# Kernel optimization log

Hardware: AMD Instinct MI355X
Metric: run time of the kernel (lower is better)

Reference implementation:

```python
import jax, jax.numpy as jnp
import numpy as np
from jax import lax

VOCAB = 32000
EMBED = 1024
HIDDEN = 1024
ML = 64          # config.MAX_LENGTH
L = 50           # input sentence length
HH = HIDDEN // 2 # per-direction encoder hidden


def _lstm_cell(x, h, c, Wih, Whh, bih, bhh):
    # torch LSTM gate order: i, f, g, o
    g = x @ Wih.T + h @ Whh.T + bih + bhh
    i, f, gg, o = jnp.split(g, 4)
    i = jax.nn.sigmoid(i)
    f = jax.nn.sigmoid(f)
    gg = jnp.tanh(gg)
    o = jax.nn.sigmoid(o)
    c = f * c + i * gg
    return o * jnp.tanh(c), c


def setup_inputs() -> dict:
    key = jax.random.key(0)
    ks = jax.random.split(key, 24)
    def n(k, shape, s=0.05):
        return jax.random.normal(k, shape, jnp.float32) * s
    return {
        "x_tokens": jax.random.randint(ks[0], (L,), 0, VOCAB, jnp.int32),
        "allowed_mask": jnp.ones((VOCAB + ML,), jnp.float32),
        "embedding": n(ks[1], (VOCAB, EMBED)),
        # encoder bi-LSTM (two cells, each hidden//2)
        "Wih_f": n(ks[2], (4 * HH, EMBED)), "Whh_f": n(ks[3], (4 * HH, HH)),
        "bih_f": n(ks[4], (4 * HH,)), "bhh_f": n(ks[5], (4 * HH,)),
        "Wih_b": n(ks[6], (4 * HH, EMBED)), "Whh_b": n(ks[7], (4 * HH, HH)),
        "bih_b": n(ks[8], (4 * HH,)), "bhh_b": n(ks[9], (4 * HH,)),
        # decoder LSTM: input = embed + 2*hidden
        "Wih_d": n(ks[10], (4 * HIDDEN, EMBED + 2 * HIDDEN)),
        "Whh_d": n(ks[11], (4 * HIDDEN, HIDDEN)),
        "bih_d": n(ks[12], (4 * HIDDEN,)), "bhh_d": n(ks[13], (4 * HIDDEN,)),
        # attention: Linear(2*hidden -> MAX_LENGTH)
        "attn_W": n(ks[14], (ML, 2 * HIDDEN)), "attn_b": n(ks[15], (ML,)),
        # generate layer: Linear(hidden -> vocab)
        "gen_W": n(ks[16], (VOCAB, HIDDEN)), "gen_b": n(ks[17], (VOCAB,)),
        # copy layer: Linear(hidden -> hidden)
        "copy_W": n(ks[18], (HIDDEN, HIDDEN)), "copy_b": n(ks[19], (HIDDEN,)),
    }


def _forward(allowed_mask, embedding, Wih_f, Whh_f, bih_f, bhh_f,
             Wih_b, Whh_b, bih_b, bhh_b, Wih_d, Whh_d, bih_d, bhh_d,
             attn_W, attn_b, gen_W, gen_b, copy_W, copy_b, x_tokens):
    xemb = embedding[x_tokens]  # (L, EMBED)

    # --- encoder: two LSTM cells both stepped forward-in-time (as in the
    # original, where the bidirectional LSTM is called one token at a time) ---
    def enc_step(carry, xe):
        hf, cf, hb, cb = carry
        hf, cf = _lstm_cell(xe, hf, cf, Wih_f, Whh_f, bih_f, bhh_f)
        hb, cb = _lstm_cell(xe, hb, cb, Wih_b, Whh_b, bih_b, bhh_b)
        return (hf, cf, hb, cb), jnp.concatenate([hf, hb])

    z = jnp.zeros((HH,), xemb.dtype)
    (hf, cf, hb, cb), enc = lax.scan(enc_step, (z, z, z, z), xemb)
    enc_outs = jnp.zeros((ML, HIDDEN), xemb.dtype).at[:L].set(enc)  # padded buffer
    h0 = jnp.concatenate([hf, hb])  # (HIDDEN,) decoder init
    c0 = jnp.concatenate([cf, cb])

    copy_enc = jnp.tanh(enc_outs @ copy_W.T + copy_b)  # (ML, HIDDEN), loop-invariant
    pos = jnp.arange(ML)
    sent_pad = jnp.full((ML,), -1, jnp.int32).at[:L].set(x_tokens)
    sos_emb = embedding[0]

    def dec_step(carry, t):
        h, c, prev_probs, prev_word, dec_in = carry
        first = t == 0
        # attentive read
        a = jnp.concatenate([dec_in, h])  # (2*HIDDEN,)
        attw = jax.nn.softmax(a @ attn_W.T + attn_b)
        attentive = attw @ enc_outs  # (HIDDEN,)
        # selective (copy) read from previous step's copy probs
        pc = prev_probs[VOCAB:]
        m = ((pos >= 1) & (pos < L - 1) & (sent_pad != prev_word)).astype(pc.dtype)
        pc = pc * m
        s = pc.sum()
        pc = jnp.where(s > 0, pc / jnp.where(s > 0, s, 1.0), pc)
        selective = pc @ enc_outs
        zero = jnp.zeros_like(attentive)
        attentive = jnp.where(first, zero, attentive)
        selective = jnp.where(first, zero, selective)
        # decoder LSTM step
        h, c = _lstm_cell(jnp.concatenate([dec_in, selective, attentive]),
                          h, c, Wih_d, Whh_d, bih_d, bhh_d)
        gen = h @ gen_W.T + gen_b        # (VOCAB,)
        copy = copy_enc @ h              # (ML,)
        probs = jax.nn.softmax(jnp.concatenate([gen, copy]))
        dist = probs * allowed_mask
        # deterministic action (argmax in place of Categorical.sample)
        aidx = jnp.argmax(dist)
        is_voc = aidx < VOCAB
        src = sent_pad[jnp.clip(aidx - VOCAB, 0, L - 1)]
        action = jnp.where(is_voc, aidx, src).astype(jnp.int32)
        prob = dist[aidx] + jnp.where(
            is_voc, jnp.zeros((), dist.dtype), dist[jnp.clip(action, 0, VOCAB - 1)])
        new = (h, c, lax.stop_gradient(probs), action, embedding[action])
        return new, (h, prob, action)

    carry0 = (h0, c0, jnp.zeros((VOCAB + ML,), h0.dtype),
              jnp.array(-1, jnp.int32), sos_emb)
    _, (hs, probs, actions) = lax.scan(dec_step, carry0, jnp.arange(ML))
    states = jnp.concatenate([h0[None], hs])  # (ML+1, HIDDEN)
    return states, probs, actions


def reference(x_tokens, allowed_mask, embedding, Wih_f, Whh_f, bih_f, bhh_f,
              Wih_b, Whh_b, bih_b, bhh_b, Wih_d, Whh_d, bih_d, bhh_d,
              attn_W, attn_b, gen_W, gen_b, copy_W, copy_b):
    return _forward(allowed_mask, embedding, Wih_f, Whh_f, bih_f, bhh_f,
                    Wih_b, Whh_b, bih_b, bhh_b, Wih_d, Whh_d, bih_d, bhh_d,
                    attn_W, attn_b, gen_W, gen_b, copy_W, copy_b, x_tokens)
```

## Files before the change

### kernel.cpp

```cpp
#include <hip/hip_runtime.h>
#include <math.h>

#define L 50
#define ML 64
#define VOCAB 32000
#define EMBED 1024
#define HID 1024
#define HH 512
#define TOT (VOCAB+ML)
#define NPART 501

#define WS_ENC_GATES 0
#define WS_C_ENC     8192
#define WS_ENC_OUTS  10240
#define WS_COPY_ENC  75776
#define WS_H_DEC     141312
#define WS_C_DEC     143360
#define WS_X_DEC     145408
#define WS_DGATES    148480
#define WS_LOGITS    152576
#define WS_PARTS     184640
#define WS_ATTW      186688
#define WS_PC        186752
#define WS_ACT       186816
#define WS_G         186880
#define WS_G_END     (186880+8192*64)
#define WS_PREG      711168
#define WS_PREG_END  (711168+50*4096)
#define WS_AH        915968
#define WS_P         916032
#define WS_P_END     (916032+32000*64)

__device__ __forceinline__ float wred_sum(float v){
  #pragma unroll
  for(int o=32;o;o>>=1) v += __shfl_xor(v,o,64);
  return v;
}
__device__ __forceinline__ float wred_max(float v){
  #pragma unroll
  for(int o=32;o;o>>=1) v = fmaxf(v,__shfl_xor(v,o,64));
  return v;
}
__device__ __forceinline__ float sigm(float x){ return 1.0f/(1.0f+__expf(-x)); }
__device__ __forceinline__ float d4(float4 a, float4 b){ return a.x*b.x + a.y*b.y + a.z*b.z + a.w*b.w; }

__global__ __launch_bounds__(256) void k_enc_pre2(
  const int* __restrict__ xt, const float* __restrict__ emb,
  const float* __restrict__ Wih_f, const float* __restrict__ bih_f, const float* __restrict__ bhh_f,
  const float* __restrict__ Wih_b, const float* __restrict__ bih_b, const float* __restrict__ bhh_b,
  float* __restrict__ ws)
{
  __shared__ int toks[L];
  const int tid=threadIdx.x, b=blockIdx.x, wave=tid>>6, lane=tid&63;
  float* pg = ws + WS_PREG;
  if(tid<L) toks[tid]=xt[tid];
  float4 wih[2][4]; float bias[2];
  #pragma unroll
  for(int rr=0;rr<2;rr++){
    int r=b*8+wave*2+rr; bool isF=(r<2048); int rl=isF?r:(r-2048);
    const float* wp=(isF?Wih_f:Wih_b)+(size_t)rl*EMBED;
    #pragma unroll
    for(int c4=0;c4<4;c4++) wih[rr][c4]=*(const float4*)(wp+c4*256+lane*4);
    bias[rr]= isF?(bih_f[rl]+bhh_f[rl]):(bih_b[rl]+bhh_b[rl]);
  }
  __syncthreads();
  const float* er0 = emb + (size_t)toks[0]*EMBED;
  float4 e0=*(const float4*)(er0      +lane*4);
  float4 e1=*(const float4*)(er0+256  +lane*4);
  float4 e2=*(const float4*)(er0+512  +lane*4);
  float4 e3=*(const float4*)(er0+768  +lane*4);
  for(int t=0;t<L;t++){
    int tn = (t+1<L)? t+1 : t;
    const float* en = emb + (size_t)toks[tn]*EMBED;
    float4 n0=*(const float4*)(en      +lane*4);
    float4 n1=*(const float4*)(en+256  +lane*4);
    float4 n2=*(const float4*)(en+512  +lane*4);
    float4 n3=*(const float4*)(en+768  +lane*4);
    #pragma unroll
    for(int rr=0;rr<2;rr++){
      int r=b*8+wave*2+rr;
      float acc = d4(wih[rr][0],e0)+d4(wih[rr][1],e1)+d4(wih[rr][2],e2)+d4(wih[rr][3],e3);
      acc=wred_sum(acc);
      if(lane==0) pg[(size_t)t*4096+r]=acc+bias[rr];
    }
    e0=n0; e1=n1; e2=n2; e3=n3;
  }
}

__global__ __launch_bounds__(256) void k_enc_rec(
  const float* __restrict__ Whh_f, const float* __restrict__ Whh_b,
  float* __restrict__ ws, int t)
{
  __shared__ __align__(16) float h_lds[1024];
  const int tid=threadIdx.x, b=blockIdx.x, wave=tid>>6, lane=tid&63;
  float* gates   = ws + WS_ENC_GATES;
  float* c_enc   = ws + WS_C_ENC;
  float* enc_outs= ws + WS_ENC_OUTS;
  const float* pg = ws + WS_PREG + (size_t)t*4096;
  if(t>0){
    const float* gp = gates + ((t-1)&1)*4096;
    const float* cp = c_enc + (t&1)*1024;
    float* cw = c_enc + ((t-1)&1)*1024;
    for(int u=tid;u<1024;u+=256){
      int base=(u<512)?0:2048, uu=(u<512)?u:(u-512);
      float ig=gp[base+uu], fg=gp[base+512+uu], gg=gp[base+1024+uu], og=gp[base+1536+uu];
      float cprev=(t==1)?0.0f:cp[u];
      float c=sigm(fg)*cprev+sigm(ig)*tanhf(gg);
      float h=sigm(og)*tanhf(c);
      h_lds[u]=h;
      if(b==0){ cw[u]=c; enc_outs[(size_t)(t-1)*1024+u]=h; }
    }
  }
  __syncthreads();
  float* gw = gates + (t&1)*4096;
  #pragma unroll
  for(int rr=0;rr<2;rr++){
    int r=b*8+wave*2+rr; bool isF=(r<2048); int rl=isF?r:(r-2048);
    if(t==0){
      if(lane==0) gw[r]=pg[r];
    } else {
      const float* hr=(isF?Whh_f:Whh_b)+(size_t)rl*HH;
      const float* hs=&h_lds[isF?0:512];
      float acc=0.0f;
      #pragma unroll
      for(int c2=0;c2<2;c2++){
        int m=c2*256+lane*4;
        acc += d4(*(const float4*)(hr+m), *(const float4*)(&hs[m]));
      }
      acc=wred_sum(acc);
      if(lane==0) gw[r]=pg[r]+acc;
    }
  }
}

__global__ __launch_bounds__(256) void k_enc_step(
  const int* __restrict__ xt, const float* __restrict__ emb,
  const float* __restrict__ Wih_f, const float* __restrict__ Whh_f,
  const float* __restrict__ bih_f, const float* __restrict__ bhh_f,
  const float* __restrict__ Wih_b, const float* __restrict__ Whh_b,
  const float* __restrict__ bih_b, const float* __restrict__ bhh_b,
  float* __restrict__ ws, int t)
{
  __shared__ __align__(16) float h_lds[1024];
  __shared__ __align__(16) float xe[1024];
  const int tid = threadIdx.x;
  float* gates   = ws + WS_ENC_GATES;
  float* c_enc   = ws + WS_C_ENC;
  float* enc_outs= ws + WS_ENC_OUTS;
  {
    const int tok = xt[t];
    const float* er = emb + (size_t)tok*EMBED;
    for(int j=tid;j<1024;j+=256) xe[j]=er[j];
  }
  if(t>0){
    const float* gp = gates + ((t-1)&1)*4096;
    const float* cp = c_enc + (t&1)*1024;
    float* cw = c_enc + ((t-1)&1)*1024;
    for(int u=tid;u<1024;u+=256){
      int base=(u<512)?0:2048, uu=(u<512)?u:(u-512);
      float ig=gp[base+uu], fg=gp[base+512+uu], gg=gp[base+1024+uu], og=gp[base+1536+uu];
      float cprev=(t==1)?0.0f:cp[u];
      float c=sigm(fg)*cprev+sigm(ig)*tanhf(gg);
      float h=sigm(og)*tanhf(c);
      h_lds[u]=h;
      if(blockIdx.x==0){ cw[u]=c; enc_outs[(size_t)(t-1)*1024+u]=h; }
    }
  }
  __syncthreads();
  float* gw = gates + (t&1)*4096;
  const int wave=tid>>6, lane=tid&63;
  for(int rr=0;rr<2;rr++){
    int r=blockIdx.x*8+wave*2+rr;
    bool isF=(r<2048); int rl=isF?r:(r-2048);
    const float* Wih=isF?Wih_f:Wih_b;
    const float* Whh=isF?Whh_f:Whh_b;
    float bias=isF?(bih_f[rl]+bhh_f[rl]):(bih_b[rl]+bhh_b[rl]);
    const float* wr=Wih+(size_t)rl*EMBED;
    float acc=0.0f;
    #pragma unroll
    for(int c4=0;c4<4;c4++){
      int m=c4*256+lane*4;
      acc += d4(*(const float4*)(wr+m), *(const float4*)(&xe[m]));
    }
    if(t>0){
      const float* hr=Whh+(size_t)rl*HH;
      const float* hs=&h_lds[isF?0:512];
      #pragma unroll
      for(int c2=0;c2<2;c2++){
        int m=c2*256+lane*4;
        acc += d4(*(const float4*)(hr+m), *(const float4*)(&hs[m]));
      }
    }
    acc=wred_sum(acc);
    if(lane==0) gw[r]=acc+bias;
  }
}

__global__ __launch_bounds__(256) void k_copy_final(
  const float* __restrict__ emb,
  const float* __restrict__ copy_W, const float* __restrict__ copy_b,
  float* __restrict__ ws, float* __restrict__ out)
{
  __shared__ __align__(16) float hf[1024];
  const int tid=threadIdx.x, b=blockIdx.x, wave=tid>>6, lane=tid&63;
  float* gates = ws + WS_ENC_GATES;
  float* c_enc = ws + WS_C_ENC;
  float* enc_outs = ws + WS_ENC_OUTS;
  float* cenc = ws + WS_COPY_ENC;
  float* h_dec = ws + WS_H_DEC;
  float* c_dec = ws + WS_C_DEC;
  float* x_dec = ws + WS_X_DEC;
  {
    const float* gp = gates + ((L-1)&1)*4096;
    const float* cp = c_enc + ((L-2)&1)*1024;
    for(int u=tid;u<1024;u+=256){
      int base=(u<512)?0:2048, uu=(u<512)?u:(u-512);
      float ig=gp[base+uu], fg=gp[base+512+uu], gg=gp[base+1024+uu], og=gp[base+1536+uu];
      float c=sigm(fg)*cp[u]+sigm(ig)*tanhf(gg);
      float h=sigm(og)*tanhf(c);
      hf[u]=h;
      if(b==0){
        enc_outs[(size_t)(L-1)*1024+u]=h;
        h_dec[1024+u]=h;
        c_dec[1024+u]=c;
        out[u]=h;
      }
    }
    if(b==1) for(int j=tid;j<(ML-L)*1024;j+=256) enc_outs[(size_t)L*1024+j]=0.0f;
    if(b==2) for(int j=tid;j<1024;j+=256){
      x_dec[j]=emb[j];
      x_dec[1024+j]=0.0f;
      x_dec[2048+j]=0.0f;
    }
  }
  __syncthreads();
  int j = b*4 + wave;
  const float* wr = copy_W + (size_t)j*1024;
  float4 w0=*(const float4*)(wr+0*256+lane*4);
  float4 w1=*(const float4*)(wr+1*256+lane*4);
  float4 w2=*(const float4*)(wr+2*256+lane*4);
  float4 w3=*(const float4*)(wr+3*256+lane*4);
  float bj = copy_b[j];
  for(int k=0;k<L-1;k++){
    const float* er = enc_outs + (size_t)k*1024;
    float acc = d4(w0,*(const float4*)(er+0*256+lane*4))
              + d4(w1,*(const float4*)(er+1*256+lane*4))
              + d4(w2,*(const float4*)(er+2*256+lane*4))
              + d4(w3,*(const float4*)(er+3*256+lane*4));
    acc = wred_sum(acc);
    if(lane==0) cenc[(size_t)k*1024+j]=tanhf(acc+bj);
  }
  {
    float acc = d4(w0,*(const float4*)(&hf[0*256+lane*4]))
              + d4(w1,*(const float4*)(&hf[1*256+lane*4]))
              + d4(w2,*(const float4*)(&hf[2*256+lane*4]))
              + d4(w3,*(const float4*)(&hf[3*256+lane*4]));
    acc = wred_sum(acc);
    if(lane==0) cenc[(size_t)(L-1)*1024+j]=tanhf(acc+bj);
  }
  if(lane==0){
    float z=tanhf(0.0f+bj);
    for(int k=L;k<ML;k++) cenc[(size_t)k*1024+j]=z;
  }
}

__global__ __launch_bounds__(256) void k_gmat3(const float* __restrict__ Wih_d, float* __restrict__ ws)
{
  const int tid=threadIdx.x, wave=tid>>6, lane=tid&63;
  const float* enc = ws + WS_ENC_OUTS;
  float* G = ws + WS_G;
  float4 w[4][4];
  int rg[4];
  #pragma unroll
  for(int q=0;q<4;q++){
    int r = blockIdx.x*16 + wave*4 + q;
    rg[q]=r;
    const float* W = (r<4096) ? (Wih_d + (size_t)r*3072 + 1024)
                              : (Wih_d + (size_t)(r-4096)*3072 + 2048);
    #pragma unroll
    for(int c4=0;c4<4;c4++) w[q][c4]=*(const float4*)(W + c4*256 + lane*4);
  }
  const float* er0 = enc;
  float4 e0=*(const float4*)(er0      +lane*4);
  float4 e1=*(const float4*)(er0+256  +lane*4);
  float4 e2=*(const float4*)(er0+512  +lane*4);
  float4 e3=*(const float4*)(er0+768  +lane*4);
  for(int k=0;k<L;k++){
    int kn = (k+1<L)? k+1 : k;
    const float* en = enc + (size_t)kn*1024;
    float4 n0=*(const float4*)(en      +lane*4);
    float4 n1=*(const float4*)(en+256  +lane*4);
    float4 n2=*(const float4*)(en+512  +lane*4);
    float4 n3=*(const float4*)(en+768  +lane*4);
    #pragma unroll
    for(int q=0;q<4;q++){
      float acc = d4(w[q][0],e0)+d4(w[q][1],e1)+d4(w[q][2],e2)+d4(w[q][3],e3);
      acc=wred_sum(acc);
      if(lane==0) G[(size_t)rg[q]*64 + k]=acc;
    }
    e0=n0; e1=n1; e2=n2; e3=n3;
  }
  if(lane==0){
    #pragma unroll
    for(int q=0;q<4;q++)
      for(int kk=L;kk<64;kk++) G[(size_t)rg[q]*64 + kk]=0.0f;
  }
}

__global__ __launch_bounds__(256) void k_pmat3(
  const float* __restrict__ emb, const float* __restrict__ attn_W, float* __restrict__ ws)
{
  const int tid=threadIdx.x, wave=tid>>6, lane=tid&63;
  float* P = ws + WS_P;
  const int w0 = (blockIdx.x>>2)*16;
  const int r0 = (blockIdx.x&3)*16 + wave*4;
  float4 w[4][4];
  #pragma unroll
  for(int q=0;q<4;q++){
    const float* wr = attn_W + (size_t)(r0+q)*2048;
    #pragma unroll
    for(int c4=0;c4<4;c4++) w[q][c4]=*(const float4*)(wr + c4*256 + lane*4);
  }
  const float* er0 = emb + (size_t)w0*EMBED;
  float4 e0=*(const float4*)(er0      +lane*4);
  float4 e1=*(const float4*)(er0+256  +lane*4);
  float4 e2=*(const float4*)(er0+512  +lane*4);
  float4 e3=*(const float4*)(er0+768  +lane*4);
  for(int wv=0;wv<16;wv++){
    int wn = (wv+1<16)? wv+1 : wv;
    const float* en = emb + (size_t)(w0+wn)*EMBED;
    float4 n0=*(const float4*)(en      +lane*4);
    float4 n1=*(const float4*)(en+256  +lane*4);
    float4 n2=*(const float4*)(en+512  +lane*4);
    float4 n3=*(const float4*)(en+768  +lane*4);
    #pragma unroll
    for(int q=0;q<4;q++){
      float acc = d4(w[q][0],e0)+d4(w[q][1],e1)+d4(w[q][2],e2)+d4(w[q][3],e3);
      acc=wred_sum(acc);
      if(lane==0) P[(size_t)(w0+wv)*64 + r0+q]=acc;
    }
    e0=n0; e1=n1; e2=n2; e3=n3;
  }
}

__global__ __launch_bounds__(256) void k_fin16(
  const int* __restrict__ xt, const float* __restrict__ amask,
  const float* __restrict__ emb,
  const float* __restrict__ attn_W, const float* __restrict__ attn_b,
  float* __restrict__ ws, float* __restrict__ out, int t, int fin_only)
{
  __shared__ __align__(16) float dec_in[1024];
  __shared__ __align__(16) float hprev[1024];
  __shared__ float r_lm[256], r_sm[256], r_ky[256];
  __shared__ int r_ix[256];
  __shared__ float s_lmax, s_Z;
  __shared__ int s_act;
  const int tid=threadIdx.x, b=blockIdx.x, wave=tid>>6, lane=tid&63;
  float* h_dec=ws+WS_H_DEC;
  float* logits=ws+WS_LOGITS; float* parts=ws+WS_PARTS;
  float* attw_raw=ws+WS_ATTW; float* pcw=ws+WS_PC;
  {
    float lm=-INFINITY, sm=0.0f, ky=-INFINITY; int ix=0x7fffffff;
    for(int i=tid;i<NPART;i+=256){
      const float4 p = *(const float4*)(parts+(size_t)i*4);
      float plm=p.x, psm=p.y, pky=p.z; int pix=__float_as_int(p.w);
      if(plm>lm){ sm = sm*__expf(lm-plm)+psm; lm=plm; }
      else sm += psm*__expf(plm-lm);
      if(pky>ky || (pky==ky && pix<ix)){ ky=pky; ix=pix; }
    }
    r_lm[tid]=lm; r_sm[tid]=sm; r_ky[tid]=ky; r_ix[tid]=ix;
    __syncthreads();
    for(int s=128;s;s>>=1){
      if(tid<s){
        float blm=r_lm[tid+s], bsm=r_sm[tid+s];
        float alm=r_lm[tid], a_sm=r_sm[tid];
        if(blm>alm){ r_sm[tid]=a_sm*__expf(alm-blm)+bsm; r_lm[tid]=blm; }
        else r_sm[tid]=a_sm+bsm*__expf(blm-alm);
        float bky=r_ky[tid+s]; int bix=r_ix[tid+s];
        if(bky>r_ky[tid] || (bky==r_ky[tid] && bix<r_ix[tid])){ r_ky[tid]=bky; r_ix[tid]=bix; }
      }
      __syncthreads();
    }
    if(tid==0){
      float lmax=r_lm[0]; float Z=r_sm[0];
      float bky=r_ky[0];
      int aidx = (bky==-INFINITY)?0:r_ix[0];
      bool isv = aidx<VOCAB;
      int kcl = aidx-VOCAB; kcl = kcl<0?0:(kcl>(L-1)?(L-1):kcl);
      int sp = xt[kcl];
      int action = isv? aidx : sp;
      if(b==0){
        float prob = amask[aidx]*__expf(logits[aidx]-lmax)/Z;
        if(!isv){
          int a2 = action<0?0:(action>(VOCAB-1)?(VOCAB-1):action);
          prob += amask[a2]*__expf(logits[a2]-lmax)/Z;
        }
        out[65*1024 + (t-1)] = prob;
        out[65*1024 + 64 + (t-1)] = (float)action;
        *(int*)(ws+WS_ACT) = action;
      }
      s_lmax=lmax; s_Z=Z; s_act=action;
    }
  }
  __syncthreads();
  if(fin_only) return;

  const int action = s_act;
  if(b==0 && tid<64){
    int k=tid;
    float v=__expf(logits[VOCAB+k]-s_lmax)/s_Z;
    int sp=(k<L)? xt[k] : -1;
    float m=(k>=1 && k<(L-1) && sp!=action)?1.0f:0.0f;
    float pv=v*m;
    float s=wred_sum(pv);
    pcw[k]=(s>0.0f)? pv/s : pv;
  }
  {
    int row = action<0 ? action+VOCAB : action;
    const float* er = emb + (size_t)row*EMBED;
    const float* hp = h_dec + ((t-1)&1)*1024;
    for(int j=tid;j<1024;j+=256){ dec_in[j]=er[j]; hprev[j]=hp[j]; }
  }
  __syncthreads();
  {
    int r = b*4 + wave;
    const float* wr = attn_W + (size_t)r*2048;
    float acc=0.0f;
    #pragma unroll
    for(int c4=0;c4<4;c4++){
      int m=c4*256+lane*4;
      acc += d4(*(const float4*)(wr+m),      *(const float4*)(&dec_in[m]));
      acc += d4(*(const float4*)(wr+1024+m), *(const float4*)(&hprev[m]));
    }
    acc=wred_sum(acc);
    if(lane==0) attw_raw[r]=acc+attn_b[r];
  }
}

__global__ __launch_bounds__(256) void k_dec_gates4(
  const int* __restrict__ xt, const float* __restrict__ amask,
  const float* __restrict__ emb, const float* __restrict__ attn_b,
  const float* __restrict__ Wih_d, const float* __restrict__ Whh_d,
  const float* __restrict__ bih_d, const float* __restrict__ bhh_d,
  float* __restrict__ ws, float* __restrict__ out, int t)
{
  __shared__ __align__(16) float di[1024];
  __shared__ __align__(16) float hh[1024];
  __shared__ float pcs[64], aws[64];
  __shared__ float r_lm[256], r_sm[256], r_ky[256];
  __shared__ int r_ix[256];
  __shared__ float s_lmax, s_Z;
  __shared__ int s_act;
  const int tid=threadIdx.x, b=blockIdx.x, wave=tid>>6, lane=tid&63;
  float* h_dec=ws+WS_H_DEC; float* dg=ws+WS_DGATES;
  float* logits=ws+WS_LOGITS; float* parts=ws+WS_PARTS;
  const float* G=ws+WS_G;

  if(t==0){
    for(int j=tid;j<1024;j+=256) di[j]=emb[j];
    if(tid<64){ pcs[tid]=0.0f; aws[tid]=0.0f; }
  } else {
    float lm=-INFINITY, sm=0.0f, ky=-INFINITY; int ix=0x7fffffff;
    for(int i=tid;i<NPART;i+=256){
      const float4 p = *(const float4*)(parts+(size_t)i*4);
      float plm=p.x, psm=p.y, pky=p.z; int pix=__float_as_int(p.w);
      if(plm>lm){ sm = sm*__expf(lm-plm)+psm; lm=plm; }
      else sm += psm*__expf(plm-lm);
      if(pky>ky || (pky==ky && pix<ix)){ ky=pky; ix=pix; }
    }
    r_lm[tid]=lm; r_sm[tid]=sm; r_ky[tid]=ky; r_ix[tid]=ix;
    __syncthreads();
    for(int s=128;s;s>>=1){
      if(tid<s){
        float blm=r_lm[tid+s], bsm=r_sm[tid+s];
        float alm=r_lm[tid], a_sm=r_sm[tid];
        if(blm>alm){ r_sm[tid]=a_sm*__expf(alm-blm)+bsm; r_lm[tid]=blm; }
        else r_sm[tid]=a_sm+bsm*__expf(blm-alm);
        float bky=r_ky[tid+s]; int bix=r_ix[tid+s];
        if(bky>r_ky[tid] || (bky==r_ky[tid] && bix<r_ix[tid])){ r_ky[tid]=bky; r_ix[tid]=bix; }
      }
      __syncthreads();
    }
    if(tid==0){
      float lmax=r_lm[0]; float Z=r_sm[0];
      float bky=r_ky[0];
      int aidx = (bky==-INFINITY)?0:r_ix[0];
      bool isv = aidx<VOCAB;
      int kcl = aidx-VOCAB; kcl = kcl<0?0:(kcl>(L-1)?(L-1):kcl);
      int sp = xt[kcl];
      int action = isv? aidx : sp;
      if(b==0){
        float prob = amask[aidx]*__expf(logits[aidx]-lmax)/Z;
        if(!isv){
          int a2 = action<0?0:(action>(VOCAB-1)?(VOCAB-1):action);
          prob += amask[a2]*__expf(logits[a2]-lmax)/Z;
        }
        out[65*1024 + (t-1)] = prob;
        out[65*1024 + 64 + (t-1)] = (float)action;
      }
      s_lmax=lmax; s_Z=Z; s_act=action;
    }
    __syncthreads();
    const int action = s_act;
    if(tid<64){
      int k=tid;
      float v=__expf(logits[VOCAB+k]-s_lmax)/s_Z;
      int sp=(k<L)? xt[k] : -1;
      float m=(k>=1 && k<(L-1) && sp!=action)?1.0f:0.0f;
      float pv=v*m;
      float s=wred_sum(pv);
      pcs[k]=(s>0.0f)? pv/s : pv;
    }
    __syncthreads();
    if(tid<64){
      float raw = (ws+WS_P)[(size_t)action*64 + tid] + (ws+WS_AH)[tid] + attn_b[tid];
      float mx=wred_max(raw);
      float e=__expf(raw-mx);
      float s=wred_sum(e);
      aws[tid]=e/s;
    }
    {
      const float* er = emb + (size_t)action*EMBED;
      for(int j=tid;j<1024;j+=256) di[j]=er[j];
    }
  }
  {
    const float* hp=h_dec+((t+1)&1)*1024;
    for(int j=tid;j<1024;j+=256) hh[j]=hp[j];
  }
  __syncthreads();
  for(int rr=0;rr<2;rr++){
    int r=b*8+wave*2+rr;
    const float* wd=Wih_d+(size_t)r*3072;
    float acc=0.0f;
    #pragma unroll
    for(int c4=0;c4<4;c4++){
      int m=c4*256+lane*4;
      acc += d4(*(const float4*)(wd+m), *(const float4*)(&di[m]));
    }
    const float* hr=Whh_d+(size_t)r*1024;
    #pragma unroll
    for(int c4=0;c4<4;c4++){
      int m=c4*256+lane*4;
      acc += d4(*(const float4*)(hr+m), *(const float4*)(&hh[m]));
    }
    acc += G[(size_t)r*64+lane]*pcs[lane];
    acc += G[(size_t)(4096+r)*64+lane]*aws[lane];
    acc=wred_sum(acc);
    if(lane==0) dg[r]=acc+bih_d[r]+bhh_d[r];
  }
}

__global__ __launch_bounds__(256) void k_dec_gates3(
  const float* __restrict__ emb,
  const float* __restrict__ Wih_d, const float* __restrict__ Whh_d,
  const float* __restrict__ bih_d, const float* __restrict__ bhh_d,
  float* __restrict__ ws, int t)
{
  __shared__ __align__(16) float di[1024];
  __shared__ __align__(16) float hh[1024];
  __shared__ float pcs[64], aws[64];
  const int tid=threadIdx.x;
  float* h_dec=ws+WS_H_DEC; float* dg=ws+WS_DGATES;
  const float* G=ws+WS_G;
  if(t==0){
    for(int j=tid;j<1024;j+=256) di[j]=emb[j];
    if(tid<64){ pcs[tid]=0.0f; aws[tid]=0.0f; }
  } else {
    const int action = *(const int*)(ws+WS_ACT);
    const float* er = emb + (size_t)action*EMBED;
    for(int j=tid;j<1024;j+=256) di[j]=er[j];
    if(tid<64){
      pcs[tid]=(ws+WS_PC)[tid];
      float v=(ws+WS_ATTW)[tid];
      float mx=wred_max(v);
      float e=__expf(v-mx);
      float s=wred_sum(e);
      aws[tid]=e/s;
    }
  }
  {
    const float* hp=h_dec+((t+1)&1)*1024;
    for(int j=tid;j<1024;j+=256) hh[j]=hp[j];
  }
  __syncthreads();
  const int wave=tid>>6, lane=tid&63;
  for(int rr=0;rr<2;rr++){
    int r=blockIdx.x*8+wave*2+rr;
    const float* wd=Wih_d+(size_t)r*3072;
    float acc=0.0f;
    #pragma unroll
    for(int c4=0;c4<4;c4++){
      int m=c4*256+lane*4;
      acc += d4(*(const float4*)(wd+m), *(const float4*)(&di[m]));
    }
    const float* hr=Whh_d+(size_t)r*1024;
    #pragma unroll
    for(int c4=0;c4<4;c4++){
      int m=c4*256+lane*4;
      acc += d4(*(const float4*)(hr+m), *(const float4*)(&hh[m]));
    }
    acc += G[(size_t)r*64+lane]*pcs[lane];
    acc += G[(size_t)(4096+r)*64+lane]*aws[lane];
    acc=wred_sum(acc);
    if(lane==0) dg[r]=acc+bih_d[r]+bhh_d[r];
  }
}

__global__ __launch_bounds__(256) void k_dec_gen2(
  const float* __restrict__ gen_W, const float* __restrict__ gen_b,
  const float* __restrict__ amask, const float* __restrict__ attn_W,
  float* __restrict__ ws, float* __restrict__ out, int t)
{
  __shared__ __align__(16) float h_lds[1024];
  __shared__ float w_lm[4], w_sm[4], w_ky[4];
  __shared__ int w_ix[4];
  const int tid=threadIdx.x;
  float* dg=ws+WS_DGATES;
  float* c_dec=ws+WS_C_DEC; float* h_dec=ws+WS_H_DEC;
  float* logits=ws+WS_LOGITS; float* parts=ws+WS_PARTS;
  float* cenc=ws+WS_COPY_ENC;
  {
    const float* cp=c_dec+((t+1)&1)*1024;
    float* cw=c_dec+(t&1)*1024;
    float* hw=h_dec+(t&1)*1024;
    for(int u=tid;u<1024;u+=256){
      float ig=dg[u], fg=dg[1024+u], gg=dg[2048+u], og=dg[3072+u];
      float c=sigm(fg)*cp[u]+sigm(ig)*tanhf(gg);
      float h=sigm(og)*tanhf(c);
      h_lds[u]=h;
      if(blockIdx.x==0){ cw[u]=c; hw[u]=h; out[(size_t)(t+1)*1024+u]=h; }
    }
  }
  __syncthreads();
  const int wave=tid>>6, lane=tid&63;
  const int b=blockIdx.x;
  if(b==501){
    float* AH=ws+WS_AH;
    for(int rr=0;rr<16;rr++){
      int r=wave*16+rr;
      const float* wr = attn_W + (size_t)r*2048 + 1024;
      float acc=0.0f;
      #pragma unroll
      for(int c4=0;c4<4;c4++){
        int m=c4*256+lane*4;
        acc += d4(*(const float4*)(wr+m), *(const float4*)(&h_lds[m]));
      }
      acc=wred_sum(acc);
      if(lane==0) AH[r]=acc;
    }
    return;
  }
  const bool isGen=(b<500);
  const int rbase = isGen ? (b*64+wave*16) : (VOCAB+wave*16);
  float lv[16];
  #pragma unroll
  for(int rr=0;rr<16;rr++){
    const float* wr = isGen ? gen_W+(size_t)(rbase+rr)*1024
                            : cenc +(size_t)(rbase-VOCAB+rr)*1024;
    float acc=0.0f;
    #pragma unroll
    for(int c4=0;c4<4;c4++){
      int m=c4*256+lane*4;
      acc += d4(*(const float4*)(wr+m), *(const float4*)(&h_lds[m]));
    }
    acc=wred_sum(acc);
    lv[rr] = isGen ? acc+gen_b[rbase+rr] : acc;
  }
  if(lane==0){
    float lm=-INFINITY, ky=-INFINITY; int ix=0;
    #pragma unroll
    for(int rr=0;rr<16;rr++){
      int gi=rbase+rr;
      logits[gi]=lv[rr];
      lm=fmaxf(lm,lv[rr]);
      float mk=amask[gi];
      float kk = (mk>0.0f)? (lv[rr]+__logf(mk)) : -INFINITY;
      if(kk>ky){ ky=kk; ix=gi; }
    }
    float sm=0.0f;
    #pragma unroll
    for(int rr=0;rr<16;rr++) sm += __expf(lv[rr]-lm);
    w_lm[wave]=lm; w_sm[wave]=sm; w_ky[wave]=ky; w_ix[wave]=ix;
  }
  __syncthreads();
  if(tid==0){
    float lm=w_lm[0], sm=w_sm[0], ky=w_ky[0]; int ix=w_ix[0];
    for(int w=1;w<4;w++){
      float blm=w_lm[w], bsm=w_sm[w];
      if(blm>lm){ sm=sm*__expf(lm-blm)+bsm; lm=blm; }
      else sm += bsm*__expf(blm-lm);
      if(w_ky[w]>ky || (w_ky[w]==ky && w_ix[w]<ix)){ ky=w_ky[w]; ix=w_ix[w]; }
    }
    float4 p; p.x=lm; p.y=sm; p.z=ky; p.w=__int_as_float(ix);
    *(float4*)(parts+(size_t)b*4)=p;
  }
}

extern "C" void kernel_launch(void* const* d_in, const int* in_sizes, int n_in,
                              void* d_out, int out_size, void* d_ws, size_t ws_size,
                              hipStream_t stream)
{
  const int*   xt     = (const int*)d_in[0];
  const float* amask  = (const float*)d_in[1];
  const float* emb    = (const float*)d_in[2];
  const float* Wih_f  = (const float*)d_in[3];
  const float* Whh_f  = (const float*)d_in[4];
  const float* bih_f  = (const float*)d_in[5];
  const float* bhh_f  = (const float*)d_in[6];
  const float* Wih_b  = (const float*)d_in[7];
  const float* Whh_b  = (const float*)d_in[8];
  const float* bih_b  = (const float*)d_in[9];
  const float* bhh_b  = (const float*)d_in[10];
  const float* Wih_d  = (const float*)d_in[11];
  const float* Whh_d  = (const float*)d_in[12];
  const float* bih_d  = (const float*)d_in[13];
  const float* bhh_d  = (const float*)d_in[14];
  const float* attn_W = (const float*)d_in[15];
  const float* attn_b = (const float*)d_in[16];
  const float* gen_W  = (const float*)d_in[17];
  const float* gen_b  = (const float*)d_in[18];
  const float* copy_W = (const float*)d_in[19];
  const float* copy_b = (const float*)d_in[20];
  float* out=(float*)d_out;
  float* ws =(float*)d_ws;

  const bool hasPreg = ws_size >= (size_t)WS_PREG_END*sizeof(float);
  const bool hasP    = ws_size >= (size_t)WS_P_END*sizeof(float);

  if(hasPreg){
    k_enc_pre2<<<512,256,0,stream>>>(xt,emb,Wih_f,bih_f,bhh_f,Wih_b,bih_b,bhh_b,ws);
    for(int t=0;t<L;t++)
      k_enc_rec<<<512,256,0,stream>>>(Whh_f,Whh_b,ws,t);
  } else {
    for(int t=0;t<L;t++)
      k_enc_step<<<512,256,0,stream>>>(xt,emb,Wih_f,Whh_f,bih_f,bhh_f,Wih_b,Whh_b,bih_b,bhh_b,ws,t);
  }
  k_copy_final<<<256,256,0,stream>>>(emb,copy_W,copy_b,ws,out);
  k_gmat3<<<512,256,0,stream>>>(Wih_d,ws);

  if(hasP){
    k_pmat3<<<8000,256,0,stream>>>(emb,attn_W,ws);
    for(int t=0;t<ML;t++){
      k_dec_gates4<<<512,256,0,stream>>>(xt,amask,emb,attn_b,Wih_d,Whh_d,bih_d,bhh_d,ws,out,t);
      k_dec_gen2  <<<502,256,0,stream>>>(gen_W,gen_b,amask,attn_W,ws,out,t);
    }
    k_fin16<<<1,256,0,stream>>>(xt,amask,emb,attn_W,attn_b,ws,out,ML,1);
  } else {
    k_dec_gates3<<<512,256,0,stream>>>(emb,Wih_d,Whh_d,bih_d,bhh_d,ws,0);
    k_dec_gen2  <<<501,256,0,stream>>>(gen_W,gen_b,amask,attn_W,ws,out,0);
    for(int t=1;t<ML;t++){
      k_fin16     <<<16,256,0,stream>>>(xt,amask,emb,attn_W,attn_b,ws,out,t,0);
      k_dec_gates3<<<512,256,0,stream>>>(emb,Wih_d,Whh_d,bih_d,bhh_d,ws,t);
      k_dec_gen2  <<<501,256,0,stream>>>(gen_W,gen_b,amask,attn_W,ws,out,t);
    }
    k_fin16<<<1,256,0,stream>>>(xt,amask,emb,attn_W,attn_b,ws,out,ML,1);
  }
}
```

Measured before the change: 3.184 ms.

## Rewrite embedding-attention precompute as LDS-tiled register-blocked GEMM

Replaces the per-row wave-reduction kernel that computes embedding times attention-weight projections with a classic shared-memory tiled GEMM. Each block handles 64 vocabulary rows against all 64 attention rows, staging 64-wide K chunks in padded LDS and accumulating a 4x4 register tile per thread. This removes the cross-lane reductions and the repeated reloading of attn_W across 8000 blocks. The cost is more synchronisation and LDS traffic, and the 4-way scalar stores into LDS may cause bank conflicts.

```diff
diff --git a/kernel.cpp b/kernel.cpp
--- a/kernel.cpp
+++ b/kernel.cpp
@@ -307,39 +307,48 @@
   }
 }
 
-__global__ __launch_bounds__(256) void k_pmat3(
+__global__ __launch_bounds__(256) void k_pmat4(
   const float* __restrict__ emb, const float* __restrict__ attn_W, float* __restrict__ ws)
 {
-  const int tid=threadIdx.x, wave=tid>>6, lane=tid&63;
+  __shared__ float e_lds[64][65];
+  __shared__ float w_lds[64][65];
+  const int tid=threadIdx.x;
+  const int wq=tid>>4, rq=tid&15;
   float* P = ws + WS_P;
-  const int w0 = (blockIdx.x>>2)*16;
-  const int r0 = (blockIdx.x&3)*16 + wave*4;
-  float4 w[4][4];
+  const int w0 = blockIdx.x*64;
+  float acc[4][4];
   #pragma unroll
-  for(int q=0;q<4;q++){
-    const float* wr = attn_W + (size_t)(r0+q)*2048;
-    #pragma unroll
-    for(int c4=0;c4<4;c4++) w[q][c4]=*(const float4*)(wr + c4*256 + lane*4);
-  }
-  const float* er0 = emb + (size_t)w0*EMBED;
-  float4 e0=*(const float4*)(er0      +lane*4);
-  float4 e1=*(const float4*)(er0+256  +lane*4);
-  float4 e2=*(const float4*)(er0+512  +lane*4);
-  float4 e3=*(const float4*)(er0+768  +lane*4);
-  for(int wv=0;wv<16;wv++){
-    int wn = (wv+1<16)? wv+1 : wv;
-    const float* en = emb + (size_t)(w0+wn)*EMBED;
-    float4 n0=*(const float4*)(en      +lane*4);
-    float4 n1=*(const float4*)(en+256  +lane*4);
-    float4 n2=*(const float4*)(en+512  +lane*4);
-    float4 n3=*(const float4*)(en+768  +lane*4);
-    #pragma unroll
-    for(int q=0;q<4;q++){
-      float acc = d4(w[q][0],e0)+d4(w[q][1],e1)+d4(w[q][2],e2)+d4(w[q][3],e3);
-      acc=wred_sum(acc);
-      if(lane==0) P[(size_t)(w0+wv)*64 + r0+q]=acc;
-    }
-    e0=n0; e1=n1; e2=n2; e3=n3;
+  for(int i=0;i<4;i++)
+    #pragma unroll
+    for(int j=0;j<4;j++) acc[i][j]=0.0f;
+  for(int kc=0;kc<16;kc++){
+    __syncthreads();
+    #pragma unroll
+    for(int v=0;v<4;v++){
+      int idx=(v*256+tid)*4;
+      int row=idx>>6, col=idx&63;
+      float4 te=*(const float4*)(emb    + (size_t)(w0+row)*EMBED + kc*64 + col);
+      e_lds[row][col]=te.x; e_lds[row][col+1]=te.y; e_lds[row][col+2]=te.z; e_lds[row][col+3]=te.w;
+      float4 tw=*(const float4*)(attn_W + (size_t)row*2048      + kc*64 + col);
+      w_lds[row][col]=tw.x; w_lds[row][col+1]=tw.y; w_lds[row][col+2]=tw.z; w_lds[row][col+3]=tw.w;
+    }
+    __syncthreads();
+    for(int kk=0;kk<64;kk++){
+      float e[4], w[4];
+      #pragma unroll
+      for(int i=0;i<4;i++) e[i]=e_lds[wq*4+i][kk];
+      #pragma unroll
+      for(int j=0;j<4;j++) w[j]=w_lds[rq*4+j][kk];
+      #pragma unroll
+      for(int i=0;i<4;i++)
+        #pragma unroll
+        for(int j=0;j<4;j++) acc[i][j] += e[i]*w[j];
+    }
+  }
+  #pragma unroll
+  for(int i=0;i<4;i++){
+    float4 st; st.x=acc[i][0]; st.y=acc[i][1]; st.z=acc[i][2]; st.w=acc[i][3];
+    *(float4*)(P + (size_t)(w0+wq*4+i)*64 + rq*4) = st;
   }
 }
 
@@ -740,7 +749,7 @@
   k_gmat3<<<512,256,0,stream>>>(Wih_d,ws);
 
   if(hasP){
-    k_pmat3<<<8000,256,0,stream>>>(emb,attn_W,ws);
+    k_pmat4<<<500,256,0,stream>>>(emb,attn_W,ws);
     for(int t=0;t<ML;t++){
       k_dec_gates4<<<512,256,0,stream>>>(xt,amask,emb,attn_b,Wih_d,Whh_d,bih_d,bhh_d,ws,out,t);
       k_dec_gen2  <<<502,256,0,stream>>>(gen_W,gen_b,amask,attn_W,ws,out,t);
```

After: 3.125 ms. About the same (-1.9%).
